# Kernel tuning notes

Measured on AMD Instinct MI355X. Metric: run time of the kernel, lower is better.

The kernel has to match this reference:

```python
import jax, jax.numpy as jnp
import numpy as np
from jax.scipy.special import logsumexp

B, S, L = 1024, 8192, 3


def setup_inputs() -> dict:
    key = jax.random.key(0)
    k1, k2, k3, k4, k5 = jax.random.split(key, 5)
    emissions = jax.random.normal(k1, (B, S, L), dtype=jnp.float32)
    labels = jax.random.randint(k2, (B, S), 0, L, dtype=jnp.int64)
    start_transitions = 0.1 * jax.random.normal(k3, (L,), dtype=jnp.float32)
    transitions = 0.1 * jax.random.normal(k4, (L, L), dtype=jnp.float32)
    end_transitions = 0.1 * jax.random.normal(k5, (L,), dtype=jnp.float32)
    return {
        "emissions": emissions,
        "labels": labels,
        "start_transitions": start_transitions,
        "transitions": transitions,
        "end_transitions": end_transitions,
    }


def reference(emissions, labels, start_transitions, transitions, end_transitions):
    # mask is all-ones in the original module, so every timestep is valid.
    # --- log partition via forward algorithm (sequential DP over time) ---
    alpha0 = start_transitions[None, :] + emissions[:, 0]  # [B, L]

    def step(alpha, e_t):
        # alpha: [B, L] (prev label), e_t: [B, L] (next label)
        nxt = logsumexp(alpha[:, :, None] + transitions[None, :, :] + e_t[:, None, :], axis=1)
        return nxt, None

    e_rest = jnp.swapaxes(emissions[:, 1:], 0, 1)  # [S-1, B, L]
    alphaT, _ = jax.lax.scan(step, alpha0, e_rest)
    log_z = logsumexp(alphaT + end_transitions[None, :], axis=-1)  # [B]

    # --- gold path score ---
    em_score = jnp.take_along_axis(emissions, labels[:, :, None], axis=2)[..., 0].sum(axis=1)  # [B]
    trans_score = transitions[labels[:, :-1], labels[:, 1:]].sum(axis=1)  # [B]
    score = start_transitions[labels[:, 0]] + em_score + trans_score + end_transitions[labels[:, -1]]

    log_likelihood = jnp.sum(score - log_z)  # torchcrf default reduction='sum'
    return -log_likelihood
```

## Files before the change

kernel.cpp:

```cpp
#include <hip/hip_runtime.h>

#define LOG2E 1.44269504088896340736f
#define LN2   0.69314718055994530942f
#define S_    8192
#define WCH   512
#define NCH   16
#define KPT   8

#if __has_builtin(__builtin_amdgcn_exp2f)
__device__ __forceinline__ float exp2f_(float x){ return __builtin_amdgcn_exp2f(x); }
#else
__device__ __forceinline__ float exp2f_(float x){ return __expf(x * LN2); }
#endif
#if __has_builtin(__builtin_amdgcn_logf)
__device__ __forceinline__ float log2f_(float x){ return __builtin_amdgcn_logf(x); }
#else
__device__ __forceinline__ float log2f_(float x){ return __logf(x) * LOG2E; }
#endif

__device__ __forceinline__ void renorm9(float* V, float& s){
    float m = fmaxf(fmaxf(fmaxf(V[0],V[1]),fmaxf(V[2],V[3])),
                    fmaxf(fmaxf(V[4],V[5]),fmaxf(V[6],V[7])));
    m = fmaxf(m, V[8]);
    int e = (__float_as_int(m) >> 23) & 0xff;
    float rs = __int_as_float((254 - e) << 23);
#pragma unroll
    for (int k=0;k<9;++k) V[k] *= rs;
    s += (float)(e - 127);
}

__device__ __forceinline__ void mul33(float* C, const float* A, const float* B){
#pragma unroll
    for (int i=0;i<3;i++){
        float a0=A[i*3], a1=A[i*3+1], a2=A[i*3+2];
#pragma unroll
        for (int j=0;j<3;j++)
            C[i*3+j] = a0*B[j] + a1*B[3+j] + a2*B[6+j];
    }
}

extern "C" __global__ __launch_bounds__(64)
void crf_fwd(const float* __restrict__ em, const int* __restrict__ lab,
             const float* __restrict__ stt, const float* __restrict__ trt,
             const float* __restrict__ ent, float* __restrict__ ws)
{
    const int bid = blockIdx.x;
    const int b = bid >> 4, h = bid & 15;
    const int ln = threadIdx.x;

    __shared__ float tT[9];

    const float* emB = em + ((size_t)b*S_ + (size_t)h*WCH)*3;
    const int*   lbB = lab + (size_t)b*S_ + h*WCH;

    const float4* ep = (const float4*)emB + ln*6;
    float4 r0=ep[0], r1=ep[1], r2=ep[2], r3=ep[3], r4=ep[4], r5=ep[5];

    const int4* lb4 = (const int4*)lbB;
    int4 lv0 = lb4[2*ln], lv1 = lb4[2*ln+1];

    if (ln < 9) tT[ln] = trt[ln];

    float W00=__expf(trt[0]), W01=__expf(trt[1]), W02=__expf(trt[2]);
    float W10=__expf(trt[3]), W11=__expf(trt[4]), W12=__expf(trt[5]);
    float W20=__expf(trt[6]), W21=__expf(trt[7]), W22=__expf(trt[8]);

    const bool head = (h==0 && ln==0);
    int prev_sh = __shfl_up(lv1.w, 1, 64);
    int prev;
    if (ln == 0) prev = head ? 0 : lbB[-1];
    else         prev = prev_sh;

    __syncthreads();

    float ew[24];
    *(float4*)&ew[0]=r0;  *(float4*)&ew[4]=r1;  *(float4*)&ew[8]=r2;
    *(float4*)&ew[12]=r3; *(float4*)&ew[16]=r4; *(float4*)&ew[20]=r5;
    int lw[8] = {lv0.x,lv0.y,lv0.z,lv0.w, lv1.x,lv1.y,lv1.z,lv1.w};

    float V[9] = {1,0,0, 0,1,0, 0,0,1};
    float S2 = 0.f, sc = 0.f;
#pragma unroll
    for (int s=0; s<KPT; ++s){
        float ea=ew[3*s], eb=ew[3*s+1], ec=ew[3*s+2];
        int l = lw[s];
        float ee = (l==1) ? eb : ((l==2) ? ec : ea);
        if (head && s==0) sc += stt[l] + ee;
        else              sc += tT[prev*3+l] + ee;
        prev = l;
        if (!(head && s==0)) {
            float E0=__expf(ea), E1=__expf(eb), E2=__expf(ec);
#pragma unroll
            for (int i=0;i<3;i++){
                float a0=V[i*3], a1=V[i*3+1], a2=V[i*3+2];
                V[i*3]  =(a0*W00+a1*W10+a2*W20)*E0;
                V[i*3+1]=(a0*W01+a1*W11+a2*W21)*E1;
                V[i*3+2]=(a0*W02+a1*W12+a2*W22)*E2;
            }
        }
        if (s==3 || s==7) renorm9(V, S2);
    }

#pragma unroll
    for (int off=1; off<64; off<<=1){
        float bv[9];
#pragma unroll
        for (int k=0;k<9;++k) bv[k] = __shfl_down(V[k], (unsigned)off, 64);
        float bs2 = __shfl_down(S2, (unsigned)off, 64);
        float C[9]; mul33(C, V, bv);
        S2 += bs2;
        renorm9(C, S2);
#pragma unroll
        for (int k=0;k<9;++k) V[k]=C[k];
    }
#pragma unroll
    for (int off=32; off; off>>=1) sc += __shfl_down(sc, (unsigned)off, 64);

    if (ln == 0){
        float* r = ws + (size_t)bid*16;
#pragma unroll
        for (int k=0;k<9;++k) r[k]=V[k];
        r[9]=S2; r[10]=sc;
        r[11]=ew[0]; r[12]=ew[1]; r[13]=ew[2];
    }
}

extern "C" __global__ __launch_bounds__(64)
void crf_fin1(const float* __restrict__ ws, const float* __restrict__ stt,
              const float* __restrict__ ent, float* __restrict__ partial)
{
    const int q = blockIdx.x*64 + threadIdx.x;
    const float* rr = ws + (size_t)q*NCH*16;
    float C[9], S = rr[9], sc = rr[10];
#pragma unroll
    for (int k=0;k<9;++k) C[k]=rr[k];
#pragma unroll
    for (int p=1;p<NCH;++p){
        const float* r = rr + p*16;
        float T[9]; mul33(T, C, r);
        S += r[9]; sc += r[10];
        renorm9(T, S);
#pragma unroll
        for (int k=0;k<9;++k) C[k]=T[k];
    }
    float a0=(stt[0]+rr[11])*LOG2E, a1=(stt[1]+rr[12])*LOG2E, a2=(stt[2]+rr[13])*LOG2E;
    float am = fmaxf(fmaxf(a0,a1),a2);
    float w0=exp2f_(a0-am), w1=exp2f_(a1-am), w2=exp2f_(a2-am);
    float q0=w0*C[0]+w1*C[3]+w2*C[6];
    float q1=w0*C[1]+w1*C[4]+w2*C[7];
    float q2=w0*C[2]+w1*C[5]+w2*C[8];
    float z = q0*exp2f_(ent[0]*LOG2E) + q1*exp2f_(ent[1]*LOG2E) + q2*exp2f_(ent[2]*LOG2E);
    float logz = (am + S + log2f_(z)) * LN2;
    float nll = logz - sc;
#pragma unroll
    for (int off=32; off; off>>=1) nll += __shfl_down(nll, (unsigned)off, 64);
    if (threadIdx.x==0) partial[blockIdx.x] = nll;
}

extern "C" __global__ __launch_bounds__(64)
void crf_fin2(const float* __restrict__ partial, float* __restrict__ out)
{
    float v = (threadIdx.x < 16) ? partial[threadIdx.x] : 0.f;
#pragma unroll
    for (int off=32; off; off>>=1) v += __shfl_down(v, (unsigned)off, 64);
    if (threadIdx.x==0) out[0] = v;
}

extern "C" void kernel_launch(void* const* d_in, const int* in_sizes, int n_in,
                              void* d_out, int out_size, void* d_ws, size_t ws_size,
                              hipStream_t stream) {
    const float* em  = (const float*)d_in[0];
    const int*   lab = (const int*)d_in[1];
    const float* stt = (const float*)d_in[2];
    const float* trt = (const float*)d_in[3];
    const float* ent = (const float*)d_in[4];
    float* out = (float*)d_out;
    float* ws  = (float*)d_ws;
    const int B = in_sizes[1] / S_;
    float* partial = ws + (size_t)NCH*B*16;

    crf_fwd<<<NCH*B, 64, 0, stream>>>(em, lab, stt, trt, ent, ws);
    crf_fin1<<<B/64, 64, 0, stream>>>(ws, stt, ent, partial);
    crf_fin2<<<1, 64, 0, stream>>>(partial, out);
}
```

Measured before the change: 184.8 us.

## Process sixteen steps per lane as two interleaved chains with packed math

Each lane now covers 16 timesteps, split into two independent 8-step matrix-product chains that are combined at the end. This adds instruction-level parallelism and halves the number of chunks (and so the shuffle-scan combines and later reduction work). The 3x3 matrices are stored as float2 pairs so multiplies can use packed FP32 ops. Labels are bit-packed into registers, and four waves share a 256-thread block. Register pressure rises from holding 48 emission values per lane, which may lower occupancy.

```diff
diff --git a/kernel.cpp b/kernel.cpp
--- a/kernel.cpp
+++ b/kernel.cpp
@@ -1,11 +1,13 @@
 #include <hip/hip_runtime.h>
+
+typedef float f32x2 __attribute__((ext_vector_type(2)));
 
 #define LOG2E 1.44269504088896340736f
 #define LN2   0.69314718055994530942f
 #define S_    8192
-#define WCH   512
-#define NCH   16
-#define KPT   8
+#define WSTEP 1024
+#define NCH   8
+#define NWAVE 4
 
 #if __has_builtin(__builtin_amdgcn_exp2f)
 __device__ __forceinline__ float exp2f_(float x){ return __builtin_amdgcn_exp2f(x); }
@@ -18,6 +20,39 @@
 __device__ __forceinline__ float log2f_(float x){ return __logf(x) * LOG2E; }
 #endif
 
+#define RNORM(L0,L1,L2,H0,H1,H2,S2) { \
+    f32x2 _m2 = __builtin_elementwise_max(__builtin_elementwise_max(L0,L1),L2); \
+    float _m  = fmaxf(fmaxf(_m2.x,_m2.y), fmaxf(fmaxf(H0,H1),H2)); \
+    int _e = (__float_as_int(_m) >> 23) & 0xff; \
+    float _rs = __int_as_float((254 - _e) << 23); \
+    L0*=_rs; L1*=_rs; L2*=_rs; H0*=_rs; H1*=_rs; H2*=_rs; \
+    S2 += (float)(_e - 127); }
+
+#define STEPM(L0,L1,L2,H0,H1,H2, ea,eb,ec) { \
+    float _E0=__expf(ea), _E1=__expf(eb), _E2=__expf(ec); \
+    f32x2 _n0=(L0*W00+L1*W10+L2*W20)*_E0; float _q0=(H0*W00+H1*W10+H2*W20)*_E0; \
+    f32x2 _n1=(L0*W01+L1*W11+L2*W21)*_E1; float _q1=(H0*W01+H1*W11+H2*W21)*_E1; \
+    f32x2 _n2=(L0*W02+L1*W12+L2*W22)*_E2; float _q2=(H0*W02+H1*W12+H2*W22)*_E2; \
+    L0=_n0; L1=_n1; L2=_n2; H0=_q0; H1=_q1; H2=_q2; }
+
+#define COMBINE(AL0,AL1,AL2,AH0,AH1,AH2, BL0,BL1,BL2,BH0,BH1,BH2) { \
+    f32x2 _c0 = AL0*BL0.x + AL1*BL0.y + AL2*BH0; \
+    float _d0 = AH0*BL0.x + AH1*BL0.y + AH2*BH0; \
+    f32x2 _c1 = AL0*BL1.x + AL1*BL1.y + AL2*BH1; \
+    float _d1 = AH0*BL1.x + AH1*BL1.y + AH2*BH1; \
+    f32x2 _c2 = AL0*BL2.x + AL1*BL2.y + AL2*BH2; \
+    float _d2 = AH0*BL2.x + AH1*BL2.y + AH2*BH2; \
+    AL0=_c0; AL1=_c1; AL2=_c2; AH0=_d0; AH1=_d1; AH2=_d2; }
+
+__device__ __forceinline__ void mul33(float* C, const float* A, const float* B){
+#pragma unroll
+    for (int i=0;i<3;i++){
+        float a0=A[i*3], a1=A[i*3+1], a2=A[i*3+2];
+#pragma unroll
+        for (int j=0;j<3;j++)
+            C[i*3+j] = a0*B[j] + a1*B[3+j] + a2*B[6+j];
+    }
+}
 __device__ __forceinline__ void renorm9(float* V, float& s){
     float m = fmaxf(fmaxf(fmaxf(V[0],V[1]),fmaxf(V[2],V[3])),
                     fmaxf(fmaxf(V[4],V[5]),fmaxf(V[6],V[7])));
@@ -29,99 +64,106 @@
     s += (float)(e - 127);
 }
 
-__device__ __forceinline__ void mul33(float* C, const float* A, const float* B){
-#pragma unroll
-    for (int i=0;i<3;i++){
-        float a0=A[i*3], a1=A[i*3+1], a2=A[i*3+2];
-#pragma unroll
-        for (int j=0;j<3;j++)
-            C[i*3+j] = a0*B[j] + a1*B[3+j] + a2*B[6+j];
-    }
-}
-
-extern "C" __global__ __launch_bounds__(64)
+extern "C" __global__ __launch_bounds__(256)
 void crf_fwd(const float* __restrict__ em, const int* __restrict__ lab,
              const float* __restrict__ stt, const float* __restrict__ trt,
              const float* __restrict__ ent, float* __restrict__ ws)
 {
-    const int bid = blockIdx.x;
-    const int b = bid >> 4, h = bid & 15;
-    const int ln = threadIdx.x;
-
-    __shared__ float tT[9];
-
-    const float* emB = em + ((size_t)b*S_ + (size_t)h*WCH)*3;
-    const int*   lbB = lab + (size_t)b*S_ + h*WCH;
-
-    const float4* ep = (const float4*)emB + ln*6;
-    float4 r0=ep[0], r1=ep[1], r2=ep[2], r3=ep[3], r4=ep[4], r5=ep[5];
-
-    const int4* lb4 = (const int4*)lbB;
-    int4 lv0 = lb4[2*ln], lv1 = lb4[2*ln+1];
-
-    if (ln < 9) tT[ln] = trt[ln];
+    const int wv = threadIdx.x >> 6, ln = threadIdx.x & 63;
+    const int g = blockIdx.x*NWAVE + wv;
+    const int b = g >> 3, h = g & 7;
+
+    __shared__ float tTw[NWAVE][12];
+    if (ln < 9) tTw[wv][ln] = trt[ln];
+
+    const float* emB = em + ((size_t)b*S_ + (size_t)h*WSTEP)*3;
+    const int*   lbB = lab + (size_t)b*S_ + h*WSTEP;
+
+    float ew[48];
+    {
+        const float4* ep = (const float4*)emB + ln*12;
+#pragma unroll
+        for (int k=0;k<12;++k){
+            float4 v = ep[k];
+            ew[4*k]=v.x; ew[4*k+1]=v.y; ew[4*k+2]=v.z; ew[4*k+3]=v.w;
+        }
+    }
+    int pa, pb, lastl;
+    {
+        const int4* lp = (const int4*)lbB + ln*4;
+        int4 a = lp[0], c = lp[1], d = lp[2], e = lp[3];
+        pa = a.x | (a.y<<2) | (a.z<<4) | (a.w<<6) | (c.x<<8) | (c.y<<10) | (c.z<<12) | (c.w<<14);
+        pb = d.x | (d.y<<2) | (d.z<<4) | (d.w<<6) | (e.x<<8) | (e.y<<10) | (e.z<<12) | (e.w<<14);
+        lastl = e.w;
+    }
 
     float W00=__expf(trt[0]), W01=__expf(trt[1]), W02=__expf(trt[2]);
     float W10=__expf(trt[3]), W11=__expf(trt[4]), W12=__expf(trt[5]);
     float W20=__expf(trt[6]), W21=__expf(trt[7]), W22=__expf(trt[8]);
-
+    float st0=stt[0], st1=stt[1], st2=stt[2];
+
+    int prevA = __shfl_up(lastl, 1, 64);
+    if (ln == 0) prevA = (h == 0) ? 0 : lbB[-1];
+    int prevB = (pa >> 14) & 3;
     const bool head = (h==0 && ln==0);
-    int prev_sh = __shfl_up(lv1.w, 1, 64);
-    int prev;
-    if (ln == 0) prev = head ? 0 : lbB[-1];
-    else         prev = prev_sh;
-
-    __syncthreads();
-
-    float ew[24];
-    *(float4*)&ew[0]=r0;  *(float4*)&ew[4]=r1;  *(float4*)&ew[8]=r2;
-    *(float4*)&ew[12]=r3; *(float4*)&ew[16]=r4; *(float4*)&ew[20]=r5;
-    int lw[8] = {lv0.x,lv0.y,lv0.z,lv0.w, lv1.x,lv1.y,lv1.z,lv1.w};
-
-    float V[9] = {1,0,0, 0,1,0, 0,0,1};
+
+    f32x2 AL0={1,0}, AL1={0,1}, AL2={0,0};  float AH0=0, AH1=0, AH2=1;
+    f32x2 BL0={1,0}, BL1={0,1}, BL2={0,0};  float BH0=0, BH1=0, BH2=1;
     float S2 = 0.f, sc = 0.f;
-#pragma unroll
-    for (int s=0; s<KPT; ++s){
-        float ea=ew[3*s], eb=ew[3*s+1], ec=ew[3*s+2];
-        int l = lw[s];
-        float ee = (l==1) ? eb : ((l==2) ? ec : ea);
-        if (head && s==0) sc += stt[l] + ee;
-        else              sc += tT[prev*3+l] + ee;
-        prev = l;
-        if (!(head && s==0)) {
-            float E0=__expf(ea), E1=__expf(eb), E2=__expf(ec);
-#pragma unroll
-            for (int i=0;i<3;i++){
-                float a0=V[i*3], a1=V[i*3+1], a2=V[i*3+2];
-                V[i*3]  =(a0*W00+a1*W10+a2*W20)*E0;
-                V[i*3+1]=(a0*W01+a1*W11+a2*W21)*E1;
-                V[i*3+2]=(a0*W02+a1*W12+a2*W22)*E2;
+
+#pragma unroll
+    for (int s=0; s<8; ++s){
+        {
+            float ea=ew[3*s], eb=ew[3*s+1], ec=ew[3*s+2];
+            int l = (pa >> (2*s)) & 3;
+            float ee = (l==1) ? eb : ((l==2) ? ec : ea);
+            if (head && s==0){
+                float sv = (l==1) ? st1 : ((l==2) ? st2 : st0);
+                sc += sv + ee;
+            } else {
+                sc += tTw[wv][prevA*3+l] + ee;
             }
-        }
-        if (s==3 || s==7) renorm9(V, S2);
-    }
+            prevA = l;
+            if (!(head && s==0)) STEPM(AL0,AL1,AL2,AH0,AH1,AH2, ea,eb,ec);
+        }
+        {
+            float ea=ew[24+3*s], eb=ew[24+3*s+1], ec=ew[24+3*s+2];
+            int l = (pb >> (2*s)) & 3;
+            float ee = (l==1) ? eb : ((l==2) ? ec : ea);
+            sc += tTw[wv][prevB*3+l] + ee;
+            prevB = l;
+            STEPM(BL0,BL1,BL2,BH0,BH1,BH2, ea,eb,ec);
+        }
+        if (s==3 || s==7){
+            RNORM(AL0,AL1,AL2,AH0,AH1,AH2, S2);
+            RNORM(BL0,BL1,BL2,BH0,BH1,BH2, S2);
+        }
+    }
+
+    COMBINE(AL0,AL1,AL2,AH0,AH1,AH2, BL0,BL1,BL2,BH0,BH1,BH2);
+    RNORM(AL0,AL1,AL2,AH0,AH1,AH2, S2);
 
 #pragma unroll
     for (int off=1; off<64; off<<=1){
-        float bv[9];
-#pragma unroll
-        for (int k=0;k<9;++k) bv[k] = __shfl_down(V[k], (unsigned)off, 64);
-        float bs2 = __shfl_down(S2, (unsigned)off, 64);
-        float C[9]; mul33(C, V, bv);
-        S2 += bs2;
-        renorm9(C, S2);
-#pragma unroll
-        for (int k=0;k<9;++k) V[k]=C[k];
+        f32x2 bL0, bL1, bL2; float bH0, bH1, bH2, bS2;
+        bL0.x=__shfl_down(AL0.x,(unsigned)off,64); bL0.y=__shfl_down(AL0.y,(unsigned)off,64);
+        bL1.x=__shfl_down(AL1.x,(unsigned)off,64); bL1.y=__shfl_down(AL1.y,(unsigned)off,64);
+        bL2.x=__shfl_down(AL2.x,(unsigned)off,64); bL2.y=__shfl_down(AL2.y,(unsigned)off,64);
+        bH0=__shfl_down(AH0,(unsigned)off,64); bH1=__shfl_down(AH1,(unsigned)off,64);
+        bH2=__shfl_down(AH2,(unsigned)off,64); bS2=__shfl_down(S2,(unsigned)off,64);
+        COMBINE(AL0,AL1,AL2,AH0,AH1,AH2, bL0,bL1,bL2,bH0,bH1,bH2);
+        S2 += bS2;
+        RNORM(AL0,AL1,AL2,AH0,AH1,AH2, S2);
     }
 #pragma unroll
     for (int off=32; off; off>>=1) sc += __shfl_down(sc, (unsigned)off, 64);
 
     if (ln == 0){
-        float* r = ws + (size_t)bid*16;
-#pragma unroll
-        for (int k=0;k<9;++k) r[k]=V[k];
-        r[9]=S2; r[10]=sc;
-        r[11]=ew[0]; r[12]=ew[1]; r[13]=ew[2];
+        float4* r = (float4*)(ws + (size_t)g*16);
+        r[0] = make_float4(AL0.x, AL1.x, AL2.x, AL0.y);
+        r[1] = make_float4(AL1.y, AL2.y, AH0,   AH1);
+        r[2] = make_float4(AH2,   S2,    sc,    ew[0]);
+        r[3] = make_float4(ew[1], ew[2], 0.f,   0.f);
     }
 }
 
@@ -179,7 +221,7 @@
     const int B = in_sizes[1] / S_;
     float* partial = ws + (size_t)NCH*B*16;
 
-    crf_fwd<<<NCH*B, 64, 0, stream>>>(em, lab, stt, trt, ent, ws);
+    crf_fwd<<<B*NCH/NWAVE, 256, 0, stream>>>(em, lab, stt, trt, ent, ws);
     crf_fin1<<<B/64, 64, 0, stream>>>(ws, stt, ent, partial);
     crf_fin2<<<1, 64, 0, stream>>>(partial, out);
 }
```

Measured after the change: 184.6 us. Within noise of the previous version (-0.1%).
